# Kernel tuning notes

Hardware: AMD Instinct MI355X
Metric: run time of the kernel (lower is better)

## Reference

```python
import jax, jax.numpy as jnp
import numpy as np

N_NODES = 100000
N_EDGES = 1600000
IN_DIM = 128
HID_DIM = 128
OUT_DIM = 2


def sage_conv(x, src, dst, deg_inv, W_l, W_r, b):
    # mean-aggregate neighbor features: messages flow src -> dst
    agg = jax.ops.segment_sum(x[src], dst, num_segments=N_NODES)  # [N, d_in]
    agg = agg * deg_inv[:, None]
    # PyG SAGEConv: out = lin_l(aggr) + lin_r(x); bias only on lin_l
    return agg @ W_l + x @ W_r + b


def setup_inputs() -> dict:
    key = jax.random.key(0)
    ks = jax.random.split(key, 9)
    x = jax.random.normal(ks[0], (N_NODES, IN_DIM), dtype=jnp.float32)
    edge_index = jax.random.randint(ks[1], (2, N_EDGES), 0, N_NODES, dtype=jnp.int64)

    def glorot(k, shape):
        lim = float(np.sqrt(6.0 / (shape[0] + shape[1])))
        return jax.random.uniform(k, shape, jnp.float32, -lim, lim)

    return {
        "x": x,
        "edge_index": edge_index,
        "W1_l": glorot(ks[2], (IN_DIM, HID_DIM)),
        "W1_r": glorot(ks[3], (IN_DIM, HID_DIM)),
        "b1": jnp.zeros((HID_DIM,), jnp.float32),
        "W2_l": glorot(ks[4], (HID_DIM, HID_DIM)),
        "W2_r": glorot(ks[5], (HID_DIM, HID_DIM)),
        "b2": jnp.zeros((HID_DIM,), jnp.float32),
        "W3_l": glorot(ks[6], (HID_DIM, OUT_DIM)),
        "W3_r": glorot(ks[7], (HID_DIM, OUT_DIM)),
        "b3": jnp.zeros((OUT_DIM,), jnp.float32),
    }


def reference(x, edge_index, W1_l, W1_r, b1, W2_l, W2_r, b2, W3_l, W3_r, b3):
    src, dst = edge_index[0], edge_index[1]
    # mean-aggregation normalization: 1/in-degree (clamped to >=1)
    deg = jax.ops.segment_sum(jnp.ones((N_EDGES,), jnp.float32), dst, num_segments=N_NODES)
    deg_inv = 1.0 / jnp.maximum(deg, 1.0)

    h = sage_conv(x, src, dst, deg_inv, W1_l, W1_r, b1)
    h = jax.nn.relu(h)  # dropout is identity in eval mode
    h = sage_conv(h, src, dst, deg_inv, W2_l, W2_r, b2)
    h = jax.nn.relu(h)
    h = sage_conv(h, src, dst, deg_inv, W3_l, W3_r, b3)
    h = jax.nn.relu(h)
    return jax.nn.log_softmax(h, axis=1)
```

## Files before the change

### kernel.cpp

```cpp
#include <hip/hip_runtime.h>
#include <math.h>

#define DIM 128

typedef __attribute__((ext_vector_type(8))) short bf16x8;
typedef __attribute__((ext_vector_type(4))) float f32x4;

__device__ __forceinline__ ushort f2bf(float f) {
  unsigned u = __float_as_uint(f);
  return (ushort)((u + 0x7FFFu + ((u >> 16) & 1u)) >> 16);
}
__device__ __forceinline__ float bf2f(ushort h) {
  return __uint_as_float(((unsigned)h) << 16);
}

__global__ __launch_bounds__(256, 5) void prep3_kernel(
    const int* __restrict__ dst, unsigned* __restrict__ deg, unsigned* __restrict__ rank, int E,
    const float* __restrict__ x,
    const float* __restrict__ W1l, const float* __restrict__ W1r,
    ushort* __restrict__ xl, ushort* __restrict__ xr,
    const float* __restrict__ W2l, const float* __restrict__ W2r,
    ushort* __restrict__ tabs, int H, int G1, int N) {
  __shared__ ushort As[128 * 32];
  __shared__ ushort Bs[64 * 32];
  const int tid = threadIdx.x;
  const int bid = blockIdx.x;
  const int r3 = bid % 3;
  const int q3 = bid / 3;

  if (r3 != 2) {
    int hid = q3 * 2 + r3;
    if (hid < H) {
      int gid = hid * 256 + tid;
      if (gid < E) rank[gid] = atomicAdd(&deg[dst[gid]], 1u);
    }
    return;
  }
  int aid = q3;
  const int TIL = 4 * G1;
  if (aid >= TIL) {
    int aid2 = aid - TIL;
    if (aid2 < 128) {
      int m = aid2 >> 6;
      const float* W = m ? W2r : W2l;
      ushort* Ht = tabs + (size_t)m * 16384;
      int idx = (aid2 & 63) * 256 + tid;
      int k = idx >> 7, n = idx & 127;
      Ht[n * DIM + k] = f2bf(W[idx]);
    }
    return;
  }

  const int m = aid / (2 * G1);
  const int rem = aid % (2 * G1);
  const int bm = (rem >> 1) * 128;
  const int bn = (rem & 1) * 64;
  const float* W = m ? W1r : W1l;
  ushort* out = m ? xr : xl;

  const int wave = tid >> 6;
  const int lane = tid & 63;
  const int l15 = lane & 15;
  const int quad = lane >> 4;

  f32x4 acc[2][4];
#pragma unroll
  for (int i = 0; i < 2; ++i)
#pragma unroll
    for (int j = 0; j < 4; ++j) acc[i][j] = (f32x4){0.f, 0.f, 0.f, 0.f};

  for (int g = 0; g < 4; ++g) {
    const int kt = g << 5;
    __syncthreads();
#pragma unroll
    for (int c = 0; c < 4; ++c) {
      int flat = c * 256 + tid;
      int row = flat >> 3;
      int q4 = flat & 7;
      int grow = bm + row;
      if (grow >= N) grow = N - 1;
      float4 v = *(const float4*)(x + (size_t)grow * DIM + kt + q4 * 4);
      int kb = q4 >> 1, ki = (q4 & 1) << 2;
      uint2 pk;
      pk.x = (unsigned)f2bf(v.x) | ((unsigned)f2bf(v.y) << 16);
      pk.y = (unsigned)f2bf(v.z) | ((unsigned)f2bf(v.w) << 16);
      *(uint2*)(&As[row * 32 + ((kb ^ (row & 3)) << 3) + ki]) = pk;
    }
#pragma unroll
    for (int c = 0; c < 8; ++c) {
      int idx = c * 256 + tid;
      int kk = idx >> 6;
      int n = idx & 63;
      Bs[n * 32 + (((kk >> 3) ^ (n & 3)) << 3) + (kk & 7)] =
          f2bf(W[(size_t)(kt + kk) * DIM + bn + n]);
    }
    __syncthreads();
    bf16x8 af[2], bfr[4];
#pragma unroll
    for (int i = 0; i < 2; ++i) {
      int ar = (wave << 5) + (i << 4) + l15;
      af[i] = *(const bf16x8*)(&As[ar * 32 + ((quad ^ (ar & 3)) << 3)]);
    }
#pragma unroll
    for (int j = 0; j < 4; ++j) {
      int br = (j << 4) + l15;
      bfr[j] = *(const bf16x8*)(&Bs[br * 32 + ((quad ^ (br & 3)) << 3)]);
    }
#pragma unroll
    for (int i = 0; i < 2; ++i)
#pragma unroll
      for (int j = 0; j < 4; ++j)
        acc[i][j] = __builtin_amdgcn_mfma_f32_16x16x32_bf16(af[i], bfr[j], acc[i][j], 0, 0, 0);
  }

#pragma unroll
  for (int i = 0; i < 2; ++i) {
#pragma unroll
    for (int r = 0; r < 4; ++r) {
      const int grow = bm + (wave << 5) + (i << 4) + (quad << 2) + r;
      if (grow < N) {
#pragma unroll
        for (int j = 0; j < 4; ++j)
          out[(size_t)grow * DIM + bn + (j << 4) + l15] = f2bf(acc[i][j][r]);
      }
    }
  }
}

__global__ __launch_bounds__(256) void scan_block_kernel(const unsigned* __restrict__ deg,
                                                         unsigned* __restrict__ excl,
                                                         unsigned* __restrict__ partial,
                                                         float* __restrict__ dinv, int N) {
  __shared__ unsigned s[256];
  int i = blockIdx.x * 256 + threadIdx.x;
  unsigned v = (i < N) ? deg[i] : 0u;
  if (i < N) dinv[i] = 1.0f / fmaxf((float)v, 1.0f);
  s[threadIdx.x] = v;
  __syncthreads();
#pragma unroll
  for (int d = 1; d < 256; d <<= 1) {
    unsigned t = (threadIdx.x >= d) ? s[threadIdx.x - d] : 0u;
    __syncthreads();
    s[threadIdx.x] += t;
    __syncthreads();
  }
  if (i < N) excl[i] = s[threadIdx.x] - v;
  if (threadIdx.x == 255) partial[blockIdx.x] = s[255];
}

__global__ __launch_bounds__(256) void scan_partials_kernel(unsigned* __restrict__ partial, int B) {
  __shared__ unsigned s[256];
  __shared__ unsigned carry;
  if (threadIdx.x == 0) carry = 0u;
  __syncthreads();
  for (int base = 0; base < B; base += 256) {
    int i = base + threadIdx.x;
    unsigned v = (i < B) ? partial[i] : 0u;
    s[threadIdx.x] = v;
    __syncthreads();
#pragma unroll
    for (int d = 1; d < 256; d <<= 1) {
      unsigned t = (threadIdx.x >= d) ? s[threadIdx.x - d] : 0u;
      __syncthreads();
      s[threadIdx.x] += t;
      __syncthreads();
    }
    if (i < B) partial[i] = carry + s[threadIdx.x] - v;
    __syncthreads();
    if (threadIdx.x == 0) carry += s[255];
    __syncthreads();
  }
}

__global__ __launch_bounds__(256) void add_offsets_kernel(const unsigned* __restrict__ excl,
                                                          const unsigned* __restrict__ partial,
                                                          unsigned* __restrict__ off, int N, int E) {
  int i = blockIdx.x * 256 + threadIdx.x;
  if (i < N) off[i] = excl[i] + partial[i >> 8];
  if (i == N) off[N] = (unsigned)E;
}

__global__ __launch_bounds__(256) void csr_fill_kernel(const int* __restrict__ src,
                                                       const int* __restrict__ dst,
                                                       const unsigned* __restrict__ rank,
                                                       const unsigned* __restrict__ off,
                                                       int* __restrict__ csr_src, int E) {
  int e = blockIdx.x * 256 + threadIdx.x;
  if (e >= E) return;
  csr_src[off[dst[e]] + rank[e]] = src[e];
}

#define GATHER_BODY(TABLE)                                                       \
  const int node = (blockIdx.x * 256 + threadIdx.x) >> 6;                        \
  if (node >= N) return;                                                         \
  const int lane = threadIdx.x & 63;                                             \
  const int eslot = lane >> 4;                                                   \
  const int col = lane & 15;                                                     \
  const unsigned beg = off[node], end = off[node + 1];                           \
  const ushort* fbase = (TABLE) + col * 8;                                       \
  float acc[8];                                                                  \
  _Pragma("unroll") for (int t = 0; t < 8; ++t) acc[t] = 0.f;                    \
  auto accum = [&](int4 v) {                                                     \
    unsigned w0 = (unsigned)v.x, w1 = (unsigned)v.y;                             \
    unsigned w2 = (unsigned)v.z, w3 = (unsigned)v.w;                             \
    acc[0] += __uint_as_float(w0 << 16);                                         \
    acc[1] += __uint_as_float(w0 & 0xFFFF0000u);                                 \
    acc[2] += __uint_as_float(w1 << 16);                                         \
    acc[3] += __uint_as_float(w1 & 0xFFFF0000u);                                 \
    acc[4] += __uint_as_float(w2 << 16);                                         \
    acc[5] += __uint_as_float(w2 & 0xFFFF0000u);                                 \
    acc[6] += __uint_as_float(w3 << 16);                                         \
    acc[7] += __uint_as_float(w3 & 0xFFFF0000u);                                 \
  };                                                                             \
  unsigned base = beg;                                                           \
  for (; base + 16 <= end; base += 16) {                                         \
    int s0 = csr_src[base + eslot];                                              \
    int s1 = csr_src[base + 4 + eslot];                                          \
    int s2 = csr_src[base + 8 + eslot];                                          \
    int s3 = csr_src[base + 12 + eslot];                                         \
    int4 v0 = *(const int4*)(fbase + (size_t)s0 * DIM);                          \
    int4 v1 = *(const int4*)(fbase + (size_t)s1 * DIM);                          \
    int4 v2 = *(const int4*)(fbase + (size_t)s2 * DIM);                          \
    int4 v3 = *(const int4*)(fbase + (size_t)s3 * DIM);                          \
    accum(v0); accum(v1); accum(v2); accum(v3);                                  \
  }                                                                              \
  for (; base + 8 <= end; base += 8) {                                           \
    int s0 = csr_src[base + eslot];                                              \
    int s1 = csr_src[base + 4 + eslot];                                          \
    int4 v0 = *(const int4*)(fbase + (size_t)s0 * DIM);                          \
    int4 v1 = *(const int4*)(fbase + (size_t)s1 * DIM);                          \
    accum(v0); accum(v1);                                                        \
  }                                                                              \
  for (unsigned e = base + eslot; e < end; e += 4) {                             \
    int s = csr_src[e];                                                          \
    int4 v = *(const int4*)(fbase + (size_t)s * DIM);                            \
    accum(v);                                                                    \
  }                                                                              \
  _Pragma("unroll") for (int t = 0; t < 8; ++t) {                                \
    acc[t] += __shfl_xor(acc[t], 32, 64);                                        \
    acc[t] += __shfl_xor(acc[t], 16, 64);                                        \
  }

__global__ __launch_bounds__(256) void gather1_kernel(
    const ushort* __restrict__ xl, const int* __restrict__ csr_src,
    const unsigned* __restrict__ off, const float* __restrict__ dinv,
    const ushort* __restrict__ xr, const float* __restrict__ b1,
    ushort* __restrict__ h1, int N) {
  GATHER_BODY(xl)
  if (eslot == 0) {
    float di = dinv[node];
    int4 xv = *(const int4*)(xr + (size_t)node * DIM + col * 8);
    float4 ba = *(const float4*)(b1 + col * 8);
    float4 bb = *(const float4*)(b1 + col * 8 + 4);
    unsigned w0 = (unsigned)xv.x, w1 = (unsigned)xv.y;
    unsigned w2 = (unsigned)xv.z, w3 = (unsigned)xv.w;
    float h[8];
    h[0] = fmaxf(acc[0] * di + __uint_as_float(w0 << 16) + ba.x, 0.f);
    h[1] = fmaxf(acc[1] * di + __uint_as_float(w0 & 0xFFFF0000u) + ba.y, 0.f);
    h[2] = fmaxf(acc[2] * di + __uint_as_float(w1 << 16) + ba.z, 0.f);
    h[3] = fmaxf(acc[3] * di + __uint_as_float(w1 & 0xFFFF0000u) + ba.w, 0.f);
    h[4] = fmaxf(acc[4] * di + __uint_as_float(w2 << 16) + bb.x, 0.f);
    h[5] = fmaxf(acc[5] * di + __uint_as_float(w2 & 0xFFFF0000u) + bb.y, 0.f);
    h[6] = fmaxf(acc[6] * di + __uint_as_float(w3 << 16) + bb.z, 0.f);
    h[7] = fmaxf(acc[7] * di + __uint_as_float(w3 & 0xFFFF0000u) + bb.w, 0.f);
    unsigned ph[4];
#pragma unroll
    for (int t = 0; t < 4; ++t)
      ph[t] = (unsigned)f2bf(h[2 * t]) | ((unsigned)f2bf(h[2 * t + 1]) << 16);
    *(int4*)(h1 + (size_t)node * DIM + col * 8) =
        make_int4((int)ph[0], (int)ph[1], (int)ph[2], (int)ph[3]);
  }
}

__global__ __launch_bounds__(256) void gemm2_kernel(
    const ushort* __restrict__ h1, const ushort* __restrict__ tabs,
    const float* __restrict__ b2, ushort* __restrict__ h1l, ushort* __restrict__ h1r,
    int G1, int N) {
  __shared__ ushort As[128 * 64];
  __shared__ ushort Bs[128 * 64];
  const int tid = threadIdx.x;
  const int m = blockIdx.x / G1;
  const int tile = blockIdx.x % G1;
  const int bm = tile * 128;
  const ushort* Wt = tabs + (size_t)m * 16384;
  ushort* out = m ? h1r : h1l;

  const int wave = tid >> 6;
  const int lane = tid & 63;
  const int l15 = lane & 15;
  const int quad = lane >> 4;
  const int wm = wave >> 1;
  const int wn = wave & 1;

  f32x4 acc[4][4];
#pragma unroll
  for (int i = 0; i < 4; ++i)
#pragma unroll
    for (int j = 0; j < 4; ++j) acc[i][j] = (f32x4){0.f, 0.f, 0.f, 0.f};

  for (int g = 0; g < 2; ++g) {
    const int kt = g << 6;
    __syncthreads();
#pragma unroll
    for (int c = 0; c < 4; ++c) {
      int flat = c * 256 + tid;
      int row = flat >> 3;
      int kg = flat & 7;
      int swz = (kg ^ (row & 7)) << 3;
      int grow = bm + row;
      if (grow >= N) grow = N - 1;
      *(int4*)(&As[row * 64 + swz]) = *(const int4*)(h1 + (size_t)grow * DIM + kt + kg * 8);
      *(int4*)(&Bs[row * 64 + swz]) = *(const int4*)(Wt + (size_t)row * DIM + kt + kg * 8);
    }
    __syncthreads();
#pragma unroll
    for (int ks = 0; ks < 2; ++ks) {
      bf16x8 af[4], bfr[4];
      int kg = (ks << 2) + quad;
#pragma unroll
      for (int i = 0; i < 4; ++i) {
        int ar = (wm << 6) + (i << 4) + l15;
        af[i] = *(const bf16x8*)(&As[ar * 64 + ((kg ^ (ar & 7)) << 3)]);
        int br = (wn << 6) + (i << 4) + l15;
        bfr[i] = *(const bf16x8*)(&Bs[br * 64 + ((kg ^ (br & 7)) << 3)]);
      }
#pragma unroll
      for (int i = 0; i < 4; ++i)
#pragma unroll
        for (int j = 0; j < 4; ++j)
          acc[i][j] = __builtin_amdgcn_mfma_f32_16x16x32_bf16(af[i], bfr[j], acc[i][j], 0, 0, 0);
    }
  }

  float bv[4];
#pragma unroll
  for (int j = 0; j < 4; ++j)
    bv[j] = m ? b2[(wn << 6) + (j << 4) + l15] : 0.f;

#pragma unroll
  for (int i = 0; i < 4; ++i) {
#pragma unroll
    for (int r = 0; r < 4; ++r) {
      const int rowl = (wm << 6) + (i << 4) + (quad << 2) + r;
      const int grow = bm + rowl;
      if (grow < N) {
#pragma unroll
        for (int j = 0; j < 4; ++j) {
          int col = (wn << 6) + (j << 4) + l15;
          out[(size_t)grow * DIM + col] = f2bf(acc[i][j][r] + bv[j]);
        }
      }
    }
  }
}

__global__ __launch_bounds__(256) void gather2_kernel(
    const ushort* __restrict__ h1l, const int* __restrict__ csr_src,
    const unsigned* __restrict__ off, const float* __restrict__ dinv,
    const ushort* __restrict__ h1r, const float* __restrict__ W3l,
    const float* __restrict__ W3r, float* __restrict__ y, int N) {
  GATHER_BODY(h1l)
  if (eslot == 0) {
    float di = dinv[node];
    int4 xv = *(const int4*)(h1r + (size_t)node * DIM + col * 8);
    unsigned w0 = (unsigned)xv.x, w1 = (unsigned)xv.y;
    unsigned w2 = (unsigned)xv.z, w3 = (unsigned)xv.w;
    float h[8];
    h[0] = fmaxf(acc[0] * di + __uint_as_float(w0 << 16), 0.f);
    h[1] = fmaxf(acc[1] * di + __uint_as_float(w0 & 0xFFFF0000u), 0.f);
    h[2] = fmaxf(acc[2] * di + __uint_as_float(w1 << 16), 0.f);
    h[3] = fmaxf(acc[3] * di + __uint_as_float(w1 & 0xFFFF0000u), 0.f);
    h[4] = fmaxf(acc[4] * di + __uint_as_float(w2 << 16), 0.f);
    h[5] = fmaxf(acc[5] * di + __uint_as_float(w2 & 0xFFFF0000u), 0.f);
    h[6] = fmaxf(acc[6] * di + __uint_as_float(w3 << 16), 0.f);
    h[7] = fmaxf(acc[7] * di + __uint_as_float(w3 & 0xFFFF0000u), 0.f);
    const int d0 = col * 8;
    float y0 = 0.f, y1 = 0.f, y2 = 0.f, y3 = 0.f;
#pragma unroll
    for (int t = 0; t < 8; t += 2) {
      float4 wl = *(const float4*)(W3l + (size_t)(d0 + t) * 2);
      float4 wr = *(const float4*)(W3r + (size_t)(d0 + t) * 2);
      y0 += h[t] * wl.x + h[t + 1] * wl.z;
      y1 += h[t] * wl.y + h[t + 1] * wl.w;
      y2 += h[t] * wr.x + h[t + 1] * wr.z;
      y3 += h[t] * wr.y + h[t + 1] * wr.w;
    }
#pragma unroll
    for (int o = 1; o < 16; o <<= 1) {
      y0 += __shfl_xor(y0, o, 64);
      y1 += __shfl_xor(y1, o, 64);
      y2 += __shfl_xor(y2, o, 64);
      y3 += __shfl_xor(y3, o, 64);
    }
    if (lane == 0) *(float4*)(y + (size_t)node * 4) = make_float4(y0, y1, y2, y3);
  }
}

__global__ __launch_bounds__(256) void final3_kernel(const float* __restrict__ y,
                                                     const int* __restrict__ csr_src,
                                                     const unsigned* __restrict__ off,
                                                     const float* __restrict__ dinv,
                                                     const float* __restrict__ b3,
                                                     float* __restrict__ out, int N) {
  int n = blockIdx.x * 256 + threadIdx.x;
  if (n >= N) return;
  unsigned beg = off[n], end = off[n + 1];
  float s0 = 0.f, s1 = 0.f;
  for (unsigned e = beg; e < end; ++e) {
    int s = csr_src[e];
    float2 v = *reinterpret_cast<const float2*>(&y[(size_t)s * 4]);
    s0 += v.x; s1 += v.y;
  }
  float di = dinv[n];
  float o0 = fmaxf(s0 * di + y[(size_t)n * 4 + 2] + b3[0], 0.f);
  float o1 = fmaxf(s1 * di + y[(size_t)n * 4 + 3] + b3[1], 0.f);
  float m = fmaxf(o0, o1);
  float l = m + logf(expf(o0 - m) + expf(o1 - m));
  out[n * 2 + 0] = o0 - l;
  out[n * 2 + 1] = o1 - l;
}

extern "C" void kernel_launch(void* const* d_in, const int* in_sizes, int n_in,
                              void* d_out, int out_size, void* d_ws, size_t ws_size,
                              hipStream_t stream) {
  const float* x   = (const float*)d_in[0];
  const int*   ei  = (const int*)d_in[1];
  const float* W1l = (const float*)d_in[2];
  const float* W1r = (const float*)d_in[3];
  const float* b1  = (const float*)d_in[4];
  const float* W2l = (const float*)d_in[5];
  const float* W2r = (const float*)d_in[6];
  const float* b2  = (const float*)d_in[7];
  const float* W3l = (const float*)d_in[8];
  const float* W3r = (const float*)d_in[9];
  const float* b3  = (const float*)d_in[10];

  const int N = in_sizes[0] / DIM;
  const int E = in_sizes[1] / 2;
  const int* src = ei;
  const int* dst = ei + E;
  const int B = (N + 255) / 256;

  char* ws = (char*)d_ws;
  size_t off_b = 0;
  auto alloc = [&](size_t bytes) {
    void* p = ws + off_b;
    off_b = (off_b + bytes + 255) & ~(size_t)255;
    return p;
  };
  unsigned* deg     = (unsigned*)alloc((size_t)N * 4);
  unsigned* excl    = (unsigned*)alloc((size_t)N * 4);
  unsigned* partial = (unsigned*)alloc((size_t)B * 4);
  unsigned* offs    = (unsigned*)alloc((size_t)(N + 1) * 4);
  unsigned* rank    = (unsigned*)alloc((size_t)E * 4);
  int*      csr_src = (int*)alloc((size_t)E * 4);
  float*    dinv    = (float*)alloc((size_t)N * 4);
  ushort*   xl      = (ushort*)alloc((size_t)N * DIM * 2);
  ushort*   xr      = (ushort*)alloc((size_t)N * DIM * 2);
  ushort*   h1      = (ushort*)alloc((size_t)N * DIM * 2);
  ushort*   tabs    = (ushort*)alloc((size_t)2 * 16384 * 2);
  float*    y       = (float*)alloc((size_t)N * 4 * 4);
  ushort* h1l = xl;
  ushort* h1r = xr;

  const int H  = (E + 255) / 256;
  const int G1 = (N + 127) / 128;
  const int AUX = 4 * G1 + 128;
  const int HQ = (H + 1) / 2;
  const int P = (AUX > HQ) ? AUX : HQ;

  hipMemsetAsync(deg, 0, (size_t)N * 4, stream);
  prep3_kernel<<<3 * P, 256, 0, stream>>>(dst, deg, rank, E, x, W1l, W1r, xl, xr,
                                          W2l, W2r, tabs, H, G1, N);

  scan_block_kernel<<<B, 256, 0, stream>>>(deg, excl, partial, dinv, N);
  scan_partials_kernel<<<1, 256, 0, stream>>>(partial, B);
  add_offsets_kernel<<<(N + 256) / 256, 256, 0, stream>>>(excl, partial, offs, N, E);
  csr_fill_kernel<<<(E + 255) / 256, 256, 0, stream>>>(src, dst, rank, offs, csr_src, E);

  const int gather_grid = (N + 3) / 4;
  gather1_kernel<<<gather_grid, 256, 0, stream>>>(xl, csr_src, offs, dinv, xr, b1, h1, N);
  gemm2_kernel<<<2 * G1, 256, 0, stream>>>(h1, tabs, b2, h1l, h1r, G1, N);
  gather2_kernel<<<gather_grid, 256, 0, stream>>>(h1l, csr_src, offs, dinv, h1r, W3l, W3r, y, N);
  final3_kernel<<<(N + 255) / 256, 256, 0, stream>>>(y, csr_src, offs, dinv, b3, (float*)d_out, N);
}
```

Measured before the change: 420.9 us.

## Reorder layer-2 as aggregate-then-GEMM and fuse CSR fill with layer-1 GEMM

```diff
diff --git a/kernel.cpp b/kernel.cpp
--- a/kernel.cpp
+++ b/kernel.cpp
@@ -14,32 +14,94 @@
   return __uint_as_float(((unsigned)h) << 16);
 }
 
-__global__ __launch_bounds__(256, 5) void prep3_kernel(
-    const int* __restrict__ dst, unsigned* __restrict__ deg, unsigned* __restrict__ rank, int E,
+__global__ __launch_bounds__(256) void hist_kernel(const int* __restrict__ dst,
+                                                   unsigned* __restrict__ deg,
+                                                   unsigned* __restrict__ rank, int E) {
+  int gid = blockIdx.x * 256 + threadIdx.x;
+  if (gid < E) rank[gid] = atomicAdd(&deg[dst[gid]], 1u);
+}
+
+__global__ __launch_bounds__(256) void scan_block_kernel(const unsigned* __restrict__ deg,
+                                                         unsigned* __restrict__ excl,
+                                                         unsigned* __restrict__ partial,
+                                                         float* __restrict__ dinv, int N) {
+  __shared__ unsigned s[256];
+  int i = blockIdx.x * 256 + threadIdx.x;
+  unsigned v = (i < N) ? deg[i] : 0u;
+  if (i < N) dinv[i] = 1.0f / fmaxf((float)v, 1.0f);
+  s[threadIdx.x] = v;
+  __syncthreads();
+#pragma unroll
+  for (int d = 1; d < 256; d <<= 1) {
+    unsigned t = (threadIdx.x >= d) ? s[threadIdx.x - d] : 0u;
+    __syncthreads();
+    s[threadIdx.x] += t;
+    __syncthreads();
+  }
+  if (i < N) excl[i] = s[threadIdx.x] - v;
+  if (threadIdx.x == 255) partial[blockIdx.x] = s[255];
+}
+
+__global__ __launch_bounds__(256) void scan_partials_kernel(unsigned* __restrict__ partial, int B) {
+  __shared__ unsigned s[256];
+  __shared__ unsigned carry;
+  if (threadIdx.x == 0) carry = 0u;
+  __syncthreads();
+  for (int base = 0; base < B; base += 256) {
+    int i = base + threadIdx.x;
+    unsigned v = (i < B) ? partial[i] : 0u;
+    s[threadIdx.x] = v;
+    __syncthreads();
+#pragma unroll
+    for (int d = 1; d < 256; d <<= 1) {
+      unsigned t = (threadIdx.x >= d) ? s[threadIdx.x - d] : 0u;
+      __syncthreads();
+      s[threadIdx.x] += t;
+      __syncthreads();
+    }
+    if (i < B) partial[i] = carry + s[threadIdx.x] - v;
+    __syncthreads();
+    if (threadIdx.x == 0) carry += s[255];
+    __syncthreads();
+  }
+}
+
+__global__ __launch_bounds__(256) void add_offsets_kernel(const unsigned* __restrict__ excl,
+                                                          const unsigned* __restrict__ partial,
+                                                          unsigned* __restrict__ off, int N, int E) {
+  int i = blockIdx.x * 256 + threadIdx.x;
+  if (i < N) off[i] = excl[i] + partial[i >> 8];
+  if (i == N) off[N] = (unsigned)E;
+}
+
+__global__ __launch_bounds__(256, 4) void gemm1_fill_kernel(
     const float* __restrict__ x,
     const float* __restrict__ W1l, const float* __restrict__ W1r,
     ushort* __restrict__ xl, ushort* __restrict__ xr,
+    const int* __restrict__ src, const int* __restrict__ dst,
+    const unsigned* __restrict__ rank, const unsigned* __restrict__ off,
+    int* __restrict__ csr_src, int E,
     const float* __restrict__ W2l, const float* __restrict__ W2r,
-    ushort* __restrict__ tabs, int H, int G1, int N) {
+    ushort* __restrict__ tabs, int F, int G1, int N) {
   __shared__ ushort As[128 * 32];
-  __shared__ ushort Bs[64 * 32];
+  __shared__ ushort Bs[128 * 32];
   const int tid = threadIdx.x;
   const int bid = blockIdx.x;
-  const int r3 = bid % 3;
-  const int q3 = bid / 3;
-
-  if (r3 != 2) {
-    int hid = q3 * 2 + r3;
-    if (hid < H) {
-      int gid = hid * 256 + tid;
-      if (gid < E) rank[gid] = atomicAdd(&deg[dst[gid]], 1u);
+  const int r5 = bid % 5;
+  const int q5 = bid / 5;
+
+  if (r5 != 4) {
+    int hid = q5 * 4 + r5;
+    if (hid < F) {
+      int e = hid * 256 + tid;
+      if (e < E) csr_src[off[dst[e]] + rank[e]] = src[e];
     }
     return;
   }
-  int aid = q3;
-  const int TIL = 4 * G1;
-  if (aid >= TIL) {
-    int aid2 = aid - TIL;
+  int aid = q5;
+  const int GEMMB = 2 * G1;
+  if (aid >= GEMMB) {
+    int aid2 = aid - GEMMB;
     if (aid2 < 128) {
       int m = aid2 >> 6;
       const float* W = m ? W2r : W2l;
@@ -51,10 +113,9 @@
     return;
   }
 
-  const int m = aid / (2 * G1);
-  const int rem = aid % (2 * G1);
-  const int bm = (rem >> 1) * 128;
-  const int bn = (rem & 1) * 64;
+  const int m = aid / G1;
+  const int tile = aid % G1;
+  const int bm = tile * 128;
   const float* W = m ? W1r : W1l;
   ushort* out = m ? xr : xl;
 
@@ -63,11 +124,11 @@
   const int l15 = lane & 15;
   const int quad = lane >> 4;
 
-  f32x4 acc[2][4];
+  f32x4 acc[2][8];
 #pragma unroll
   for (int i = 0; i < 2; ++i)
 #pragma unroll
-    for (int j = 0; j < 4; ++j) acc[i][j] = (f32x4){0.f, 0.f, 0.f, 0.f};
+    for (int j = 0; j < 8; ++j) acc[i][j] = (f32x4){0.f, 0.f, 0.f, 0.f};
 
   for (int g = 0; g < 4; ++g) {
     const int kt = g << 5;
@@ -87,30 +148,28 @@
       *(uint2*)(&As[row * 32 + ((kb ^ (row & 3)) << 3) + ki]) = pk;
     }
 #pragma unroll
-    for (int c = 0; c < 8; ++c) {
+    for (int c = 0; c < 16; ++c) {
       int idx = c * 256 + tid;
-      int kk = idx >> 6;
-      int n = idx & 63;
+      int kk = idx >> 7;
+      int n = idx & 127;
       Bs[n * 32 + (((kk >> 3) ^ (n & 3)) << 3) + (kk & 7)] =
-          f2bf(W[(size_t)(kt + kk) * DIM + bn + n]);
-    }
-    __syncthreads();
-    bf16x8 af[2], bfr[4];
+          f2bf(W[(size_t)(kt + kk) * DIM + n]);
+    }
+    __syncthreads();
+    bf16x8 af[2];
 #pragma unroll
     for (int i = 0; i < 2; ++i) {
       int ar = (wave << 5) + (i << 4) + l15;
       af[i] = *(const bf16x8*)(&As[ar * 32 + ((quad ^ (ar & 3)) << 3)]);
     }
 #pragma unroll
-    for (int j = 0; j < 4; ++j) {
+    for (int j = 0; j < 8; ++j) {
       int br = (j << 4) + l15;
-      bfr[j] = *(const bf16x8*)(&Bs[br * 32 + ((quad ^ (br & 3)) << 3)]);
-    }
-#pragma unroll
-    for (int i = 0; i < 2; ++i)
-#pragma unroll
-      for (int j = 0; j < 4; ++j)
-        acc[i][j] = __builtin_amdgcn_mfma_f32_16x16x32_bf16(af[i], bfr[j], acc[i][j], 0, 0, 0);
+      bf16x8 bfr = *(const bf16x8*)(&Bs[br * 32 + ((quad ^ (br & 3)) << 3)]);
+#pragma unroll
+      for (int i = 0; i < 2; ++i)
+        acc[i][j] = __builtin_amdgcn_mfma_f32_16x16x32_bf16(af[i], bfr, acc[i][j], 0, 0, 0);
+    }
   }
 
 #pragma unroll
@@ -120,74 +179,11 @@
       const int grow = bm + (wave << 5) + (i << 4) + (quad << 2) + r;
       if (grow < N) {
 #pragma unroll
-        for (int j = 0; j < 4; ++j)
-          out[(size_t)grow * DIM + bn + (j << 4) + l15] = f2bf(acc[i][j][r]);
+        for (int j = 0; j < 8; ++j)
+          out[(size_t)grow * DIM + (j << 4) + l15] = f2bf(acc[i][j][r]);
       }
     }
   }
-}
-
-__global__ __launch_bounds__(256) void scan_block_kernel(const unsigned* __restrict__ deg,
-                                                         unsigned* __restrict__ excl,
-                                                         unsigned* __restrict__ partial,
-                                                         float* __restrict__ dinv, int N) {
-  __shared__ unsigned s[256];
-  int i = blockIdx.x * 256 + threadIdx.x;
-  unsigned v = (i < N) ? deg[i] : 0u;
-  if (i < N) dinv[i] = 1.0f / fmaxf((float)v, 1.0f);
-  s[threadIdx.x] = v;
-  __syncthreads();
-#pragma unroll
-  for (int d = 1; d < 256; d <<= 1) {
-    unsigned t = (threadIdx.x >= d) ? s[threadIdx.x - d] : 0u;
-    __syncthreads();
-    s[threadIdx.x] += t;
-    __syncthreads();
-  }
-  if (i < N) excl[i] = s[threadIdx.x] - v;
-  if (threadIdx.x == 255) partial[blockIdx.x] = s[255];
-}
-
-__global__ __launch_bounds__(256) void scan_partials_kernel(unsigned* __restrict__ partial, int B) {
-  __shared__ unsigned s[256];
-  __shared__ unsigned carry;
-  if (threadIdx.x == 0) carry = 0u;
-  __syncthreads();
-  for (int base = 0; base < B; base += 256) {
-    int i = base + threadIdx.x;
-    unsigned v = (i < B) ? partial[i] : 0u;
-    s[threadIdx.x] = v;
-    __syncthreads();
-#pragma unroll
-    for (int d = 1; d < 256; d <<= 1) {
-      unsigned t = (threadIdx.x >= d) ? s[threadIdx.x - d] : 0u;
-      __syncthreads();
-      s[threadIdx.x] += t;
-      __syncthreads();
-    }
-    if (i < B) partial[i] = carry + s[threadIdx.x] - v;
-    __syncthreads();
-    if (threadIdx.x == 0) carry += s[255];
-    __syncthreads();
-  }
-}
-
-__global__ __launch_bounds__(256) void add_offsets_kernel(const unsigned* __restrict__ excl,
-                                                          const unsigned* __restrict__ partial,
-                                                          unsigned* __restrict__ off, int N, int E) {
-  int i = blockIdx.x * 256 + threadIdx.x;
-  if (i < N) off[i] = excl[i] + partial[i >> 8];
-  if (i == N) off[N] = (unsigned)E;
-}
-
-__global__ __launch_bounds__(256) void csr_fill_kernel(const int* __restrict__ src,
-                                                       const int* __restrict__ dst,
-                                                       const unsigned* __restrict__ rank,
-                                                       const unsigned* __restrict__ off,
-                                                       int* __restrict__ csr_src, int E) {
-  int e = blockIdx.x * 256 + threadIdx.x;
-  if (e >= E) return;
-  csr_src[off[dst[e]] + rank[e]] = src[e];
 }
 
 #define GATHER_BODY(TABLE)                                                       \
@@ -272,19 +268,34 @@
   }
 }
 
-__global__ __launch_bounds__(256) void gemm2_kernel(
-    const ushort* __restrict__ h1, const ushort* __restrict__ tabs,
-    const float* __restrict__ b2, ushort* __restrict__ h1l, ushort* __restrict__ h1r,
-    int G1, int N) {
+__global__ __launch_bounds__(256) void gather_wave_kernel(
+    const ushort* __restrict__ featH, const int* __restrict__ csr_src,
+    const unsigned* __restrict__ off, const float* __restrict__ dinv,
+    ushort* __restrict__ aggH, int N) {
+  GATHER_BODY(featH)
+  if (eslot == 0) {
+    float di = dinv[node];
+    unsigned ph[4];
+#pragma unroll
+    for (int t = 0; t < 4; ++t) {
+      ph[t] = (unsigned)f2bf(acc[2 * t] * di) | ((unsigned)f2bf(acc[2 * t + 1] * di) << 16);
+    }
+    *(int4*)(aggH + (size_t)node * DIM + col * 8) =
+        make_int4((int)ph[0], (int)ph[1], (int)ph[2], (int)ph[3]);
+  }
+}
+
+__global__ __launch_bounds__(256) void sage_mfma_kernel(
+    const ushort* __restrict__ aggH, const ushort* xH,
+    const ushort* __restrict__ WlH, const ushort* __restrict__ WrH,
+    const float* __restrict__ bias,
+    const float* __restrict__ W3l, const float* __restrict__ W3r,
+    ushort* __restrict__ outH, float* __restrict__ y, int N) {
   __shared__ ushort As[128 * 64];
   __shared__ ushort Bs[128 * 64];
+
   const int tid = threadIdx.x;
-  const int m = blockIdx.x / G1;
-  const int tile = blockIdx.x % G1;
-  const int bm = tile * 128;
-  const ushort* Wt = tabs + (size_t)m * 16384;
-  ushort* out = m ? h1r : h1l;
-
+  const int bm = blockIdx.x * 128;
   const int wave = tid >> 6;
   const int lane = tid & 63;
   const int l15 = lane & 15;
@@ -298,8 +309,10 @@
 #pragma unroll
     for (int j = 0; j < 4; ++j) acc[i][j] = (f32x4){0.f, 0.f, 0.f, 0.f};
 
-  for (int g = 0; g < 2; ++g) {
-    const int kt = g << 6;
+  for (int g = 0; g < 4; ++g) {
+    const ushort* Ap = (g < 2) ? aggH : xH;
+    const ushort* Wp = (g < 2) ? WlH : WrH;
+    const int kt = (g & 1) << 6;
     __syncthreads();
 #pragma unroll
     for (int c = 0; c < 4; ++c) {
@@ -309,8 +322,8 @@
       int swz = (kg ^ (row & 7)) << 3;
       int grow = bm + row;
       if (grow >= N) grow = N - 1;
-      *(int4*)(&As[row * 64 + swz]) = *(const int4*)(h1 + (size_t)grow * DIM + kt + kg * 8);
-      *(int4*)(&Bs[row * 64 + swz]) = *(const int4*)(Wt + (size_t)row * DIM + kt + kg * 8);
+      *(int4*)(&As[row * 64 + swz]) = *(const int4*)(Ap + (size_t)grow * DIM + kt + kg * 8);
+      *(int4*)(&Bs[row * 64 + swz]) = *(const int4*)(Wp + (size_t)row * DIM + kt + kg * 8);
     }
     __syncthreads();
 #pragma unroll
@@ -332,10 +345,21 @@
     }
   }
 
+  __syncthreads();
+  float* WcF = reinterpret_cast<float*>(As);
+  float* YpF = reinterpret_cast<float*>(As) + 512;
+
+  if (W3l) {
+    for (int t = tid; t < 512; t += 256) {
+      int col = t >> 2, c = t & 3;
+      WcF[t] = (c < 2) ? W3l[col * 2 + c] : W3r[col * 2 + (c - 2)];
+    }
+    __syncthreads();
+  }
+
   float bv[4];
 #pragma unroll
-  for (int j = 0; j < 4; ++j)
-    bv[j] = m ? b2[(wn << 6) + (j << 4) + l15] : 0.f;
+  for (int j = 0; j < 4; ++j) bv[j] = bias[(wn << 6) + (j << 4) + l15];
 
 #pragma unroll
   for (int i = 0; i < 4; ++i) {
@@ -343,56 +367,45 @@
     for (int r = 0; r < 4; ++r) {
       const int rowl = (wm << 6) + (i << 4) + (quad << 2) + r;
       const int grow = bm + rowl;
-      if (grow < N) {
-#pragma unroll
-        for (int j = 0; j < 4; ++j) {
-          int col = (wn << 6) + (j << 4) + l15;
-          out[(size_t)grow * DIM + col] = f2bf(acc[i][j][r] + bv[j]);
+      float p0 = 0.f, p1 = 0.f, p2 = 0.f, p3 = 0.f;
+#pragma unroll
+      for (int j = 0; j < 4; ++j) {
+        int col = (wn << 6) + (j << 4) + l15;
+        float v = fmaxf(acc[i][j][r] + bv[j], 0.f);
+        ushort h = f2bf(v);
+        if (outH && grow < N) outH[(size_t)grow * DIM + col] = h;
+        if (W3l) {
+          float qv = bf2f(h);
+          p0 += qv * WcF[col * 4 + 0];
+          p1 += qv * WcF[col * 4 + 1];
+          p2 += qv * WcF[col * 4 + 2];
+          p3 += qv * WcF[col * 4 + 3];
         }
       }
-    }
-  }
-}
-
-__global__ __launch_bounds__(256) void gather2_kernel(
-    const ushort* __restrict__ h1l, const int* __restrict__ csr_src,
-    const unsigned* __restrict__ off, const float* __restrict__ dinv,
-    const ushort* __restrict__ h1r, const float* __restrict__ W3l,
-    const float* __restrict__ W3r, float* __restrict__ y, int N) {
-  GATHER_BODY(h1l)
-  if (eslot == 0) {
-    float di = dinv[node];
-    int4 xv = *(const int4*)(h1r + (size_t)node * DIM + col * 8);
-    unsigned w0 = (unsigned)xv.x, w1 = (unsigned)xv.y;
-    unsigned w2 = (unsigned)xv.z, w3 = (unsigned)xv.w;
-    float h[8];
-    h[0] = fmaxf(acc[0] * di + __uint_as_float(w0 << 16), 0.f);
-    h[1] = fmaxf(acc[1] * di + __uint_as_float(w0 & 0xFFFF0000u), 0.f);
-    h[2] = fmaxf(acc[2] * di + __uint_as_float(w1 << 16), 0.f);
-    h[3] = fmaxf(acc[3] * di + __uint_as_float(w1 & 0xFFFF0000u), 0.f);
-    h[4] = fmaxf(acc[4] * di + __uint_as_float(w2 << 16), 0.f);
-    h[5] = fmaxf(acc[5] * di + __uint_as_float(w2 & 0xFFFF0000u), 0.f);
-    h[6] = fmaxf(acc[6] * di + __uint_as_float(w3 << 16), 0.f);
-    h[7] = fmaxf(acc[7] * di + __uint_as_float(w3 & 0xFFFF0000u), 0.f);
-    const int d0 = col * 8;
-    float y0 = 0.f, y1 = 0.f, y2 = 0.f, y3 = 0.f;
-#pragma unroll
-    for (int t = 0; t < 8; t += 2) {
-      float4 wl = *(const float4*)(W3l + (size_t)(d0 + t) * 2);
-      float4 wr = *(const float4*)(W3r + (size_t)(d0 + t) * 2);
-      y0 += h[t] * wl.x + h[t + 1] * wl.z;
-      y1 += h[t] * wl.y + h[t + 1] * wl.w;
-      y2 += h[t] * wr.x + h[t + 1] * wr.z;
-      y3 += h[t] * wr.y + h[t + 1] * wr.w;
-    }
-#pragma unroll
-    for (int o = 1; o < 16; o <<= 1) {
-      y0 += __shfl_xor(y0, o, 64);
-      y1 += __shfl_xor(y1, o, 64);
-      y2 += __shfl_xor(y2, o, 64);
-      y3 += __shfl_xor(y3, o, 64);
-    }
-    if (lane == 0) *(float4*)(y + (size_t)node * 4) = make_float4(y0, y1, y2, y3);
+      if (W3l) {
+#pragma unroll
+        for (int o = 1; o < 16; o <<= 1) {
+          p0 += __shfl_xor(p0, o, 64);
+          p1 += __shfl_xor(p1, o, 64);
+          p2 += __shfl_xor(p2, o, 64);
+          p3 += __shfl_xor(p3, o, 64);
+        }
+        if (l15 == 0) {
+          YpF[(rowl * 4 + 0) * 2 + wn] = p0;
+          YpF[(rowl * 4 + 1) * 2 + wn] = p1;
+          YpF[(rowl * 4 + 2) * 2 + wn] = p2;
+          YpF[(rowl * 4 + 3) * 2 + wn] = p3;
+        }
+      }
+    }
+  }
+
+  if (W3l) {
+    __syncthreads();
+    for (int t = tid; t < 512; t += 256) {
+      int grow = bm + (t >> 2);
+      if (grow < N) y[(size_t)grow * 4 + (t & 3)] = YpF[t * 2 + 0] + YpF[t * 2 + 1];
+    }
   }
 }
 
@@ -460,27 +473,32 @@
   ushort*   h1      = (ushort*)alloc((size_t)N * DIM * 2);
   ushort*   tabs    = (ushort*)alloc((size_t)2 * 16384 * 2);
   float*    y       = (float*)alloc((size_t)N * 4 * 4);
-  ushort* h1l = xl;
-  ushort* h1r = xr;
-
-  const int H  = (E + 255) / 256;
+  ushort* aggH = xl;
+
+  const int F  = (E + 255) / 256;
   const int G1 = (N + 127) / 128;
-  const int AUX = 4 * G1 + 128;
-  const int HQ = (H + 1) / 2;
-  const int P = (AUX > HQ) ? AUX : HQ;
+  const int GEMMB = 2 * G1;
+  const int AUXN = GEMMB + 128;
+  const int FQ = (F + 3) / 4;
+  const int P = (AUXN > FQ) ? AUXN : FQ;
 
   hipMemsetAsync(deg, 0, (size_t)N * 4, stream);
-  prep3_kernel<<<3 * P, 256, 0, stream>>>(dst, deg, rank, E, x, W1l, W1r, xl, xr,
-                                          W2l, W2r, tabs, H, G1, N);
-
+  hist_kernel<<<F, 256, 0, stream>>>(dst, deg, rank, E);
   scan_block_kernel<<<B, 256, 0, stream>>>(deg, excl, partial, dinv, N);
   scan_partials_kernel<<<1, 256, 0, stream>>>(partial, B);
   add_offsets_kernel<<<(N + 256) / 256, 256, 0, stream>>>(excl, partial, offs, N, E);
-  csr_fill_kernel<<<(E + 255) / 256, 256, 0, stream>>>(src, dst, rank, offs, csr_src, E);
-
+  gemm1_fill_kernel<<<5 * P, 256, 0, stream>>>(x, W1l, W1r, xl, xr,
+                                               src, dst, rank, offs, csr_src, E,
+                                               W2l, W2r, tabs, F, G1, N);
+
+  const ushort* W2lH = tabs;
+  const ushort* W2rH = tabs + 16384;
+  const int G = (N + 127) / 128;
   const int gather_grid = (N + 3) / 4;
+
   gather1_kernel<<<gather_grid, 256, 0, stream>>>(xl, csr_src, offs, dinv, xr, b1, h1, N);
-  gemm2_kernel<<<2 * G1, 256, 0, stream>>>(h1, tabs, b2, h1l, h1r, G1, N);
-  gather2_kernel<<<gather_grid, 256, 0, stream>>>(h1l, csr_src, offs, dinv, h1r, W3l, W3r, y, N);
+  gather_wave_kernel<<<gather_grid, 256, 0, stream>>>(h1, csr_src, offs, dinv, aggH, N);
+  sage_mfma_kernel<<<G, 256, 0, stream>>>(aggH, h1, W2lH, W2rH, b2,
+                                          W3l, W3r, nullptr, y, N);
   final3_kernel<<<(N + 255) / 256, 256, 0, stream>>>(y, csr_src, offs, dinv, b3, (float*)d_out, N);
 }
```

After: 465.5 us. 1.11x slower.
